# Performance work log

Measured on AMD Instinct MI355X. Metric: run time of the kernel, lower is better.

The kernel has to match this reference:

```python
import jax, jax.numpy as jnp
import numpy as np

N_NODES = 100000
N_EDGES = 3200000


def setup_inputs() -> dict:
    key = jax.random.key(0)
    ks = jax.random.split(key, 16)
    inp = {
        "noisy_coords": jax.random.normal(ks[0], (N_NODES, 3), dtype=jnp.float32),
        "atom_types": jax.random.randint(ks[1], (N_NODES,), 0, 2),
        "edge_index": jax.random.randint(ks[2], (2, N_EDGES), 0, N_NODES),
        "emb": jax.random.normal(ks[3], (2, 3), dtype=jnp.float32),
    }
    # GCNConv weights: 6->32->64->64->32->3 (hidden_dim=64)
    dims = [(6, 32), (32, 64), (64, 64), (64, 32), (32, 3)]
    for i, (din, dout) in enumerate(dims, start=1):
        inp[f"W{i}"] = jax.random.normal(ks[3 + i], (din, dout), dtype=jnp.float32) / np.sqrt(din).astype(np.float32)
        inp[f"b{i}"] = jnp.zeros((dout,), dtype=jnp.float32)
    return inp


def _gcn_conv(x, W, b, src, dst, norm, n):
    # GCNConv: X @ W, then symmetric-normalized scatter-add over edges, then bias.
    h = x @ W                       # [N, dout]
    msg = h[src] * norm[:, None]    # gather + edge normalization  [E+N, dout]
    return jax.ops.segment_sum(msg, dst, num_segments=n) + b


def reference(noisy_coords, atom_types, edge_index, emb,
              W1, b1, W2, b2, W3, b3, W4, b4, W5, b5):
    n = noisy_coords.shape[0]
    loop = jnp.arange(n)
    # PyG GCNConv adds self loops and uses deg^{-1/2} (A+I) deg^{-1/2} normalization
    src = jnp.concatenate([edge_index[0], loop])
    dst = jnp.concatenate([edge_index[1], loop])
    deg = jax.ops.segment_sum(jnp.ones(src.shape[0], dtype=jnp.float32), dst, num_segments=n)
    dinv = jnp.where(deg > 0, jax.lax.rsqrt(deg), 0.0)
    norm = dinv[src] * dinv[dst]    # [E+N]

    x = jnp.concatenate([noisy_coords, emb[atom_types]], axis=1)  # [N, 6]
    x = jax.nn.relu(_gcn_conv(x, W1, b1, src, dst, norm, n))
    x = jax.nn.relu(_gcn_conv(x, W2, b2, src, dst, norm, n))
    x = jax.nn.relu(_gcn_conv(x, W3, b3, src, dst, norm, n))
    x = jax.nn.relu(_gcn_conv(x, W4, b4, src, dst, norm, n))
    x = _gcn_conv(x, W5, b5, src, dst, norm, n)  # final layer: no relu
    return x
```

## Files before the change

kernel.cpp:

```cpp
#include <hip/hip_runtime.h>
#include <hip/hip_fp16.h>

#define NBLK_BIN 256
#define NBKT 196
#define BWIN 512
#define CAP 128


typedef unsigned int uint;

union U32H2 { uint u; __half2 h; };

__device__ inline float2 h2_to_f2(uint u) {
    U32H2 c; c.u = u;
    return __half22float2(c.h);
}
__device__ inline uint f2_to_h2(float a, float b) {
    U32H2 c; c.h = __floats2half2_rn(a, b);
    return c.u;
}

__global__ __launch_bounds__(1024) void bin_kernel(const int* __restrict__ src,
                                                   const int* __restrict__ dst,
                                                   uint* __restrict__ pairs,
                                                   int* __restrict__ blkcnt, int e) {
    __shared__ int lcnt[NBKT];
    int blk = blockIdx.x, tid = threadIdx.x;
    for (int t = tid; t < NBKT; t += 1024) lcnt[t] = 0;
    __syncthreads();
    int chunk = (e + NBLK_BIN - 1) / NBLK_BIN;
    int base = blk * chunk;
    int end = min(e, base + chunk);
    for (int i = base + tid; i < end; i += 1024) {
        int s = src[i], d = dst[i];
        int b = d >> 9;
        int pos = atomicAdd(&lcnt[b], 1);
        if (pos < CAP)
            pairs[((size_t)blk * NBKT + b) * CAP + pos] = ((uint)s << 9) | ((uint)d & 511u);
    }
    __syncthreads();
    for (int t = tid; t < NBKT; t += 1024) blkcnt[blk * NBKT + t] = min(lcnt[t], CAP);
}

__global__ __launch_bounds__(1024) void fill_kernel(const uint* __restrict__ pairs,
                                                    const int* __restrict__ blkcnt,
                                                    int* __restrict__ srcs,
                                                    int* __restrict__ cnt,
                                                    int* __restrict__ rowptr,
                                                    float* __restrict__ dinv, int n) {
    __shared__ int lc[BWIN];
    __shared__ int ps[BWIN];
    __shared__ int sm[NBLK_BIN];
    __shared__ int gbase_s;
    int b = blockIdx.x, tid = threadIdx.x;
    if (tid < BWIN) lc[tid] = 0;
    for (int t = tid; t < NBLK_BIN; t += 1024) sm[t] = blkcnt[t * NBKT + b];
    if (tid == 0) gbase_s = 0;
    __syncthreads();
    {
        long long tot = (long long)NBLK_BIN * b;
        int lsum = 0;
        for (long long j = tid; j < tot; j += 1024) {
            int blk = (int)(j / b);
            int bp  = (int)(j - (long long)blk * b);
            lsum += blkcnt[blk * NBKT + bp];
        }
        for (int o = 32; o > 0; o >>= 1) lsum += __shfl_down(lsum, o, 64);
        if ((tid & 63) == 0 && lsum != 0) atomicAdd(&gbase_s, lsum);
    }
    int wave = tid >> 6, lane = tid & 63;
    for (int blk = wave; blk < NBLK_BIN; blk += 16) {
        int m = sm[blk];
        const uint* p = pairs + ((size_t)blk * NBKT + b) * CAP;
        for (int i = lane; i < m; i += 64) atomicAdd(&lc[p[i] & 511u], 1);
    }
    __syncthreads();
    int myc = (tid < BWIN) ? lc[tid] : 0;
    if (tid < BWIN) ps[tid] = myc;
    __syncthreads();
    for (int off = 1; off < BWIN; off <<= 1) {
        int t = 0;
        if (tid < BWIN && tid >= off) t = ps[tid - off];
        __syncthreads();
        if (tid < BWIN) ps[tid] += t;
        __syncthreads();
    }
    int gbase = gbase_s;
    if (tid < BWIN) {
        int ex = ps[tid] - myc;
        int vtx = (b << 9) + tid;
        if (vtx < n) {
            cnt[vtx] = myc;
            rowptr[vtx] = gbase + ex;
            dinv[vtx] = rsqrtf(1.0f + (float)myc);
        }
    }
    __syncthreads();
    if (tid < BWIN) lc[tid] = ps[tid] - myc;
    __syncthreads();
    for (int blk = wave; blk < NBLK_BIN; blk += 16) {
        int m = sm[blk];
        const uint* p = pairs + ((size_t)blk * NBKT + b) * CAP;
        for (int i = lane; i < m; i += 64) {
            uint e2 = p[i];
            int o = atomicAdd(&lc[e2 & 511u], 1);
            srcs[gbase + o] = (int)(e2 >> 9);
        }
    }
}


__global__ __launch_bounds__(256) void build_x0_h_kernel(const float* __restrict__ coords,
                                                         const int* __restrict__ at,
                                                         const float* __restrict__ emb,
                                                         const float* __restrict__ dinv,
                                                         uint* __restrict__ x, int n) {
    int v = blockIdx.x * 256 + threadIdx.x;
    if (v >= n) return;
    float dv = dinv[v];
    float c0 = coords[3 * v + 0] * dv;
    float c1 = coords[3 * v + 1] * dv;
    float c2 = coords[3 * v + 2] * dv;
    int t = at[v];
    float e0 = emb[3 * t + 0] * dv;
    float e1 = emb[3 * t + 1] * dv;
    float e2 = emb[3 * t + 2] * dv;
    uint* row = x + (size_t)v * 4;
    row[0] = f2_to_h2(c0, c1);
    row[1] = f2_to_h2(c2, e0);
    row[2] = f2_to_h2(e1, e2);
    row[3] = 0;
}

template <int TPN, bool HAS_BIAS, bool RELU>
__global__ __launch_bounds__(256) void agg_v4_kernel(const uint* __restrict__ in_,
                                                     const float* __restrict__ dinv,
                                                     const int* __restrict__ rowptr,
                                                     const int* __restrict__ cnt,
                                                     const int* __restrict__ srcs,
                                                     const float* __restrict__ bias,
                                                     uint* __restrict__ out_, int n) {
    const uint4* in = (const uint4*)in_;
    uint4* out = (uint4*)out_;
    int gid = blockIdx.x * 256 + threadIdx.x;
    int v = gid / TPN, q = gid % TPN;
    if (v >= n) return;
    float ax[4], ay[4];
    {
        uint4 s0 = in[(size_t)v * TPN + q];
        uint su[4] = {s0.x, s0.y, s0.z, s0.w};
#pragma unroll
        for (int u = 0; u < 4; ++u) { float2 f = h2_to_f2(su[u]); ax[u] = f.x; ay[u] = f.y; }
    }
    int start = rowptr[v];
    int len = cnt[v];
    int k = 0;
    for (; k + 8 <= len; k += 8) {
        int sA = srcs[start + k];
        int sB = srcs[start + k + 1];
        int sC = srcs[start + k + 2];
        int sD = srcs[start + k + 3];
        int sE = srcs[start + k + 4];
        int sF = srcs[start + k + 5];
        int sG = srcs[start + k + 6];
        int sH = srcs[start + k + 7];
        uint4 fA = in[(size_t)sA * TPN + q];
        uint4 fB = in[(size_t)sB * TPN + q];
        uint4 fC = in[(size_t)sC * TPN + q];
        uint4 fD = in[(size_t)sD * TPN + q];
        uint4 fE = in[(size_t)sE * TPN + q];
        uint4 fF = in[(size_t)sF * TPN + q];
        uint4 fG = in[(size_t)sG * TPN + q];
        uint4 fH = in[(size_t)sH * TPN + q];
        uint ua[4] = {fA.x, fA.y, fA.z, fA.w};
        uint ub[4] = {fB.x, fB.y, fB.z, fB.w};
        uint uc[4] = {fC.x, fC.y, fC.z, fC.w};
        uint ud[4] = {fD.x, fD.y, fD.z, fD.w};
        uint ue[4] = {fE.x, fE.y, fE.z, fE.w};
        uint uf[4] = {fF.x, fF.y, fF.z, fF.w};
        uint ug[4] = {fG.x, fG.y, fG.z, fG.w};
        uint uh[4] = {fH.x, fH.y, fH.z, fH.w};
#pragma unroll
        for (int u = 0; u < 4; ++u) {
            float2 a = h2_to_f2(ua[u]);
            float2 b = h2_to_f2(ub[u]);
            float2 c = h2_to_f2(uc[u]);
            float2 d = h2_to_f2(ud[u]);
            float2 e2 = h2_to_f2(ue[u]);
            float2 f = h2_to_f2(uf[u]);
            float2 g = h2_to_f2(ug[u]);
            float2 h = h2_to_f2(uh[u]);
            ax[u] += ((a.x + b.x) + (c.x + d.x)) + ((e2.x + f.x) + (g.x + h.x));
            ay[u] += ((a.y + b.y) + (c.y + d.y)) + ((e2.y + f.y) + (g.y + h.y));
        }
    }
    for (; k + 4 <= len; k += 4) {
        int sA = srcs[start + k];
        int sB = srcs[start + k + 1];
        int sC = srcs[start + k + 2];
        int sD = srcs[start + k + 3];
        uint4 fA = in[(size_t)sA * TPN + q];
        uint4 fB = in[(size_t)sB * TPN + q];
        uint4 fC = in[(size_t)sC * TPN + q];
        uint4 fD = in[(size_t)sD * TPN + q];
        uint ua[4] = {fA.x, fA.y, fA.z, fA.w};
        uint ub[4] = {fB.x, fB.y, fB.z, fB.w};
        uint uc[4] = {fC.x, fC.y, fC.z, fC.w};
        uint ud[4] = {fD.x, fD.y, fD.z, fD.w};
#pragma unroll
        for (int u = 0; u < 4; ++u) {
            float2 a = h2_to_f2(ua[u]);
            float2 b = h2_to_f2(ub[u]);
            float2 c = h2_to_f2(uc[u]);
            float2 d = h2_to_f2(ud[u]);
            ax[u] += (a.x + b.x) + (c.x + d.x);
            ay[u] += (a.y + b.y) + (c.y + d.y);
        }
    }
    for (; k < len; ++k) {
        int s = srcs[start + k];
        uint4 f = in[(size_t)s * TPN + q];
        uint uu[4] = {f.x, f.y, f.z, f.w};
#pragma unroll
        for (int u = 0; u < 4; ++u) { float2 t = h2_to_f2(uu[u]); ax[u] += t.x; ay[u] += t.y; }
    }
    float dv = dinv[v];
#pragma unroll
    for (int u = 0; u < 4; ++u) {
        ax[u] *= dv; ay[u] *= dv;
        if (HAS_BIAS) { ax[u] += bias[8 * q + 2 * u]; ay[u] += bias[8 * q + 2 * u + 1]; }
        if (RELU) { ax[u] = fmaxf(ax[u], 0.0f); ay[u] = fmaxf(ay[u], 0.0f); }
    }
    uint4 o;
    o.x = f2_to_h2(ax[0], ay[0]);
    o.y = f2_to_h2(ax[1], ay[1]);
    o.z = f2_to_h2(ax[2], ay[2]);
    o.w = f2_to_h2(ax[3], ay[3]);
    out[(size_t)v * TPN + q] = o;
}

__global__ __launch_bounds__(256) void agg_l4l5_kernel(const uint* __restrict__ in_,
                                                       const float* __restrict__ dinv,
                                                       const int* __restrict__ rowptr,
                                                       const int* __restrict__ cnt,
                                                       const int* __restrict__ srcs,
                                                       const float* __restrict__ b4,
                                                       const float* __restrict__ W5,
                                                       float* __restrict__ outf, int n) {
    const uint4* in = (const uint4*)in_;
    int gid = blockIdx.x * 256 + threadIdx.x;
    int v = gid >> 2, q = gid & 3;
    if (v >= n) return;
    float ax[4], ay[4];
    {
        uint4 s0 = in[(size_t)v * 4 + q];
        uint su[4] = {s0.x, s0.y, s0.z, s0.w};
#pragma unroll
        for (int u = 0; u < 4; ++u) { float2 f = h2_to_f2(su[u]); ax[u] = f.x; ay[u] = f.y; }
    }
    int start = rowptr[v];
    int len = cnt[v];
    int k = 0;
    for (; k + 8 <= len; k += 8) {
        int sA = srcs[start + k];
        int sB = srcs[start + k + 1];
        int sC = srcs[start + k + 2];
        int sD = srcs[start + k + 3];
        int sE = srcs[start + k + 4];
        int sF = srcs[start + k + 5];
        int sG = srcs[start + k + 6];
        int sH = srcs[start + k + 7];
        uint4 fA = in[(size_t)sA * 4 + q];
        uint4 fB = in[(size_t)sB * 4 + q];
        uint4 fC = in[(size_t)sC * 4 + q];
        uint4 fD = in[(size_t)sD * 4 + q];
        uint4 fE = in[(size_t)sE * 4 + q];
        uint4 fF = in[(size_t)sF * 4 + q];
        uint4 fG = in[(size_t)sG * 4 + q];
        uint4 fH = in[(size_t)sH * 4 + q];
        uint ua[4] = {fA.x, fA.y, fA.z, fA.w};
        uint ub[4] = {fB.x, fB.y, fB.z, fB.w};
        uint uc[4] = {fC.x, fC.y, fC.z, fC.w};
        uint ud[4] = {fD.x, fD.y, fD.z, fD.w};
        uint ue[4] = {fE.x, fE.y, fE.z, fE.w};
        uint uf[4] = {fF.x, fF.y, fF.z, fF.w};
        uint ug[4] = {fG.x, fG.y, fG.z, fG.w};
        uint uh[4] = {fH.x, fH.y, fH.z, fH.w};
#pragma unroll
        for (int u = 0; u < 4; ++u) {
            float2 a = h2_to_f2(ua[u]);
            float2 b = h2_to_f2(ub[u]);
            float2 c = h2_to_f2(uc[u]);
            float2 d = h2_to_f2(ud[u]);
            float2 e2 = h2_to_f2(ue[u]);
            float2 f = h2_to_f2(uf[u]);
            float2 g = h2_to_f2(ug[u]);
            float2 h = h2_to_f2(uh[u]);
            ax[u] += ((a.x + b.x) + (c.x + d.x)) + ((e2.x + f.x) + (g.x + h.x));
            ay[u] += ((a.y + b.y) + (c.y + d.y)) + ((e2.y + f.y) + (g.y + h.y));
        }
    }
    for (; k + 4 <= len; k += 4) {
        int sA = srcs[start + k];
        int sB = srcs[start + k + 1];
        int sC = srcs[start + k + 2];
        int sD = srcs[start + k + 3];
        uint4 fA = in[(size_t)sA * 4 + q];
        uint4 fB = in[(size_t)sB * 4 + q];
        uint4 fC = in[(size_t)sC * 4 + q];
        uint4 fD = in[(size_t)sD * 4 + q];
        uint ua[4] = {fA.x, fA.y, fA.z, fA.w};
        uint ub[4] = {fB.x, fB.y, fB.z, fB.w};
        uint uc[4] = {fC.x, fC.y, fC.z, fC.w};
        uint ud[4] = {fD.x, fD.y, fD.z, fD.w};
#pragma unroll
        for (int u = 0; u < 4; ++u) {
            float2 a = h2_to_f2(ua[u]);
            float2 b = h2_to_f2(ub[u]);
            float2 c = h2_to_f2(uc[u]);
            float2 d = h2_to_f2(ud[u]);
            ax[u] += (a.x + b.x) + (c.x + d.x);
            ay[u] += (a.y + b.y) + (c.y + d.y);
        }
    }
    for (; k < len; ++k) {
        int s = srcs[start + k];
        uint4 f = in[(size_t)s * 4 + q];
        uint uu[4] = {f.x, f.y, f.z, f.w};
#pragma unroll
        for (int u = 0; u < 4; ++u) { float2 t = h2_to_f2(uu[u]); ax[u] += t.x; ay[u] += t.y; }
    }
    float dv = dinv[v];
    float feat[8];
#pragma unroll
    for (int u = 0; u < 4; ++u) {
        float fx = ax[u] * dv + b4[8 * q + 2 * u];
        float fy = ay[u] * dv + b4[8 * q + 2 * u + 1];
        feat[2 * u]     = fmaxf(fx, 0.0f);
        feat[2 * u + 1] = fmaxf(fy, 0.0f);
    }
    float p0 = 0.f, p1 = 0.f, p2 = 0.f;
#pragma unroll
    for (int m = 0; m < 8; ++m) {
        int j = 8 * q + m;
        p0 = fmaf(feat[m], W5[j * 3 + 0], p0);
        p1 = fmaf(feat[m], W5[j * 3 + 1], p1);
        p2 = fmaf(feat[m], W5[j * 3 + 2], p2);
    }
#pragma unroll
    for (int m = 1; m < 4; m <<= 1) {
        p0 += __shfl_xor(p0, m, 4);
        p1 += __shfl_xor(p1, m, 4);
        p2 += __shfl_xor(p2, m, 4);
    }
    float o = (q == 0) ? p0 : (q == 1 ? p1 : (q == 2 ? p2 : 0.0f));
    outf[(size_t)v * 4 + q] = (q < 3) ? o * dv : 0.0f;
}

template <int DIN, int DOUT, int DOUTH2, bool HAS_BIAS, bool RELU, bool SCALE>
__global__ __launch_bounds__(256) void gemm_h_kernel(const uint* __restrict__ xin,
                                                     const float* __restrict__ W,
                                                     const float* __restrict__ bias,
                                                     const float* __restrict__ dinv,
                                                     uint* __restrict__ xout,
                                                     int istride_u, int ostride, int n) {
    __shared__ float wlds[DIN * DOUT];
    for (int i = threadIdx.x; i < DIN * DOUT; i += 256) wlds[i] = W[i];
    __syncthreads();
    int gid = blockIdx.x * 256 + threadIdx.x;
    int v = gid / DOUTH2, j2 = gid % DOUTH2;
    if (v >= n) return;
    int j1 = 2 * j2;
    const uint* xr = xin + (size_t)v * istride_u;
    float acc0 = 0.0f, acc1 = 0.0f;
#pragma unroll
    for (int ku = 0; ku < DIN / 2; ++ku) {
        float2 xf = h2_to_f2(xr[ku]);
        int k = 2 * ku;
        acc0 = fmaf(xf.x, wlds[k * DOUT + j1], acc0);
        acc0 = fmaf(xf.y, wlds[(k + 1) * DOUT + j1], acc0);
        if (j1 + 1 < DOUT) {
            acc1 = fmaf(xf.x, wlds[k * DOUT + j1 + 1], acc1);
            acc1 = fmaf(xf.y, wlds[(k + 1) * DOUT + j1 + 1], acc1);
        }
    }
    if (HAS_BIAS) {
        acc0 += bias[j1];
        if (j1 + 1 < DOUT) acc1 += bias[j1 + 1];
    }
    if (RELU) { acc0 = fmaxf(acc0, 0.0f); acc1 = fmaxf(acc1, 0.0f); }
    if (SCALE) { float dv = dinv[v]; acc0 *= dv; acc1 *= dv; }
    xout[(size_t)v * ostride + j2] = f2_to_h2(acc0, acc1);
}

#define G34_NODES 16
__global__ __launch_bounds__(256) void gemm34_kernel(const uint* __restrict__ xin,
                                                     const float* __restrict__ W3,
                                                     const float* __restrict__ b3,
                                                     const float* __restrict__ W4,
                                                     const float* __restrict__ dinv,
                                                     uint* __restrict__ xout,
                                                     int n) {
    __shared__ float4 w3c[16][64];
    __shared__ float4 w4c[16][32];
    __shared__ float4 hb4[16][17];
    for (int idx = threadIdx.x; idx < 16 * 64; idx += 256) {
        int kc = idx >> 6, c = idx & 63;
        w3c[kc][c] = make_float4(W3[(4 * kc + 0) * 64 + c], W3[(4 * kc + 1) * 64 + c],
                                 W3[(4 * kc + 2) * 64 + c], W3[(4 * kc + 3) * 64 + c]);
    }
    for (int idx = threadIdx.x; idx < 16 * 32; idx += 256) {
        int kc = idx >> 5, c = idx & 31;
        w4c[kc][c] = make_float4(W4[(4 * kc + 0) * 32 + c], W4[(4 * kc + 1) * 32 + c],
                                 W4[(4 * kc + 2) * 32 + c], W4[(4 * kc + 3) * 32 + c]);
    }
    __syncthreads();
    int i  = threadIdx.x >> 4;
    int j2 = threadIdx.x & 15;
    int v  = blockIdx.x * G34_NODES + i;
    bool ok = (v < n);

    float acc[4] = {0.f, 0.f, 0.f, 0.f};
    if (ok) {
        const uint4* xr = (const uint4*)(xin + (size_t)v * 32);
        for (int kb = 0; kb < 8; ++kb) {
            uint4 xa = xr[kb];
            float2 f0 = h2_to_f2(xa.x);
            float2 f1 = h2_to_f2(xa.y);
            float2 f2v = h2_to_f2(xa.z);
            float2 f3 = h2_to_f2(xa.w);
            float xf0 = f0.x, xf1 = f0.y, xf2 = f1.x, xf3 = f1.y;
            float xf4 = f2v.x, xf5 = f2v.y, xf6 = f3.x, xf7 = f3.y;
#pragma unroll
            for (int u = 0; u < 4; ++u) {
                int c = j2 + 16 * u;
                float4 wa = w3c[2 * kb][c];
                float4 wb = w3c[2 * kb + 1][c];
                acc[u] = fmaf(xf0, wa.x, acc[u]);
                acc[u] = fmaf(xf1, wa.y, acc[u]);
                acc[u] = fmaf(xf2, wa.z, acc[u]);
                acc[u] = fmaf(xf3, wa.w, acc[u]);
                acc[u] = fmaf(xf4, wb.x, acc[u]);
                acc[u] = fmaf(xf5, wb.y, acc[u]);
                acc[u] = fmaf(xf6, wb.z, acc[u]);
                acc[u] = fmaf(xf7, wb.w, acc[u]);
            }
        }
    }
#pragma unroll
    for (int u = 0; u < 4; ++u) {
        int c = j2 + 16 * u;
        float h = ok ? fmaxf(acc[u] + b3[c], 0.0f) : 0.0f;
        ((float*)hb4)[i * 68 + c] = h;
    }
    __syncthreads();

    float a0 = 0.f, a1 = 0.f;
#pragma unroll
    for (int kc = 0; kc < 16; ++kc) {
        float4 h4  = hb4[i][kc];
        float4 wlo = w4c[kc][j2];
        float4 whi = w4c[kc][j2 + 16];
        a0 = fmaf(h4.x, wlo.x, a0);
        a0 = fmaf(h4.y, wlo.y, a0);
        a0 = fmaf(h4.z, wlo.z, a0);
        a0 = fmaf(h4.w, wlo.w, a0);
        a1 = fmaf(h4.x, whi.x, a1);
        a1 = fmaf(h4.y, whi.y, a1);
        a1 = fmaf(h4.z, whi.z, a1);
        a1 = fmaf(h4.w, whi.w, a1);
    }
    if (ok) {
        float dv = dinv[v];
        __half* o = (__half*)(xout + (size_t)v * 16);
        o[j2]      = __float2half(a0 * dv);
        o[j2 + 16] = __float2half(a1 * dv);
    }
}

__global__ __launch_bounds__(256) void agg_f4_kernel(const float* __restrict__ in_,
                                                     const float* __restrict__ dinv,
                                                     const int* __restrict__ rowptr,
                                                     const int* __restrict__ cnt,
                                                     const int* __restrict__ srcs,
                                                     const float* __restrict__ b,
                                                     float* __restrict__ out, int n) {
    const float4* in = (const float4*)in_;
    int v = blockIdx.x * 256 + threadIdx.x;
    if (v >= n) return;
    float4 s = in[v];
    float a0 = s.x, a1 = s.y, a2 = s.z;
    int start = rowptr[v];
    int len = cnt[v];
    int k = 0;
    for (; k + 8 <= len; k += 8) {
        int sA = srcs[start + k];
        int sB = srcs[start + k + 1];
        int sC = srcs[start + k + 2];
        int sD = srcs[start + k + 3];
        int sE = srcs[start + k + 4];
        int sF = srcs[start + k + 5];
        int sG = srcs[start + k + 6];
        int sH = srcs[start + k + 7];
        float4 fA = in[sA];
        float4 fB = in[sB];
        float4 fC = in[sC];
        float4 fD = in[sD];
        float4 fE = in[sE];
        float4 fF = in[sF];
        float4 fG = in[sG];
        float4 fH = in[sH];
        a0 += ((fA.x + fB.x) + (fC.x + fD.x)) + ((fE.x + fF.x) + (fG.x + fH.x));
        a1 += ((fA.y + fB.y) + (fC.y + fD.y)) + ((fE.y + fF.y) + (fG.y + fH.y));
        a2 += ((fA.z + fB.z) + (fC.z + fD.z)) + ((fE.z + fF.z) + (fG.z + fH.z));
    }
    for (; k + 4 <= len; k += 4) {
        int sA = srcs[start + k];
        int sB = srcs[start + k + 1];
        int sC = srcs[start + k + 2];
        int sD = srcs[start + k + 3];
        float4 fA = in[sA];
        float4 fB = in[sB];
        float4 fC = in[sC];
        float4 fD = in[sD];
        a0 += (fA.x + fB.x) + (fC.x + fD.x);
        a1 += (fA.y + fB.y) + (fC.y + fD.y);
        a2 += (fA.z + fB.z) + (fC.z + fD.z);
    }
    for (; k < len; ++k) {
        float4 f = in[srcs[start + k]];
        a0 += f.x; a1 += f.y; a2 += f.z;
    }
    float dv = dinv[v];
    out[(size_t)v * 3 + 0] = a0 * dv + b[0];
    out[(size_t)v * 3 + 1] = a1 * dv + b[1];
    out[(size_t)v * 3 + 2] = a2 * dv + b[2];
}


extern "C" void kernel_launch(void* const* d_in, const int* in_sizes, int n_in,
                              void* d_out, int out_size, void* d_ws, size_t ws_size,
                              hipStream_t stream) {
    const float* coords = (const float*)d_in[0];
    const int* at       = (const int*)d_in[1];
    const int* ei       = (const int*)d_in[2];
    const float* emb    = (const float*)d_in[3];
    const float* W1 = (const float*)d_in[4];  const float* b1 = (const float*)d_in[5];
    const float* W2 = (const float*)d_in[6];  const float* b2 = (const float*)d_in[7];
    const float* W3 = (const float*)d_in[8];  const float* b3 = (const float*)d_in[9];
    const float* W4 = (const float*)d_in[10]; const float* b4 = (const float*)d_in[11];
    const float* W5 = (const float*)d_in[12]; const float* b5 = (const float*)d_in[13];
    float* out = (float*)d_out;

    const int n = in_sizes[0] / 3;
    const int e = in_sizes[2] / 2;
    const int* src = ei;
    const int* dst = ei + e;

    char* ws = (char*)d_ws;
    size_t off = 0;
    float* dinv   = (float*)(ws + off); off += (size_t)n * 4;
    int*   cnt    = (int*)(ws + off);   off += (size_t)n * 4;
    int*   rowptr = (int*)(ws + off);   off += (size_t)n * 4;
    int*   blkcnt = (int*)(ws + off);   off += (size_t)NBLK_BIN * NBKT * 4;
    int*   srcs   = (int*)(ws + off);   off += (size_t)e * 4;
    char*  alias  = ws + off;
    uint*  pairs  = (uint*)alias;
    uint*  A_h    = (uint*)alias;
    uint*  B_h    = A_h + (size_t)n * 32;
    float* B_f    = (float*)(B_h + (size_t)n * 32);

    int nb = (n + 255) / 256;

    bin_kernel<<<NBLK_BIN, 1024, 0, stream>>>(src, dst, pairs, blkcnt, e);
    fill_kernel<<<NBKT, 1024, 0, stream>>>(pairs, blkcnt, srcs, cnt, rowptr, dinv, n);

    build_x0_h_kernel<<<nb, 256, 0, stream>>>(coords, at, emb, dinv, A_h, n);

    auto blocks = [](long long threads) { return (int)((threads + 255) / 256); };

    agg_v4_kernel<1, false, false><<<blocks((long long)n), 256, 0, stream>>>(
        A_h, dinv, rowptr, cnt, srcs, nullptr, B_h, n);
    gemm_h_kernel<6, 32, 16, true, true, true><<<blocks((long long)n * 16), 256, 0, stream>>>(
        B_h, W1, b1, dinv, A_h, 4, 16, n);

    agg_v4_kernel<4, false, false><<<blocks((long long)n * 4), 256, 0, stream>>>(
        A_h, dinv, rowptr, cnt, srcs, nullptr, B_h, n);
    gemm_h_kernel<32, 64, 32, true, true, true><<<blocks((long long)n * 32), 256, 0, stream>>>(
        B_h, W2, b2, dinv, A_h, 16, 32, n);

    agg_v4_kernel<8, false, false><<<blocks((long long)n * 8), 256, 0, stream>>>(
        A_h, dinv, rowptr, cnt, srcs, nullptr, B_h, n);
    gemm34_kernel<<<(n + G34_NODES - 1) / G34_NODES, 256, 0, stream>>>(
        B_h, W3, b3, W4, dinv, A_h, n);

    agg_l4l5_kernel<<<blocks((long long)n * 4), 256, 0, stream>>>(
        A_h, dinv, rowptr, cnt, srcs, b4, W5, B_f, n);

    agg_f4_kernel<<<blocks((long long)n), 256, 0, stream>>>(
        B_f, dinv, rowptr, cnt, srcs, b5, out, n);
}
```

Baseline: 387.5 us.

## Sort nodes by degree with counting sort to balance aggregation wavefronts

Result: slower. 787.9 us (+103.3%).

```diff
diff --git a/kernel.cpp b/kernel.cpp
--- a/kernel.cpp
+++ b/kernel.cpp
@@ -5,6 +5,7 @@
 #define NBKT 196
 #define BWIN 512
 #define CAP 128
+#define DBINS 256
 
 
 typedef unsigned int uint;
@@ -107,6 +108,37 @@
             srcs[gbase + o] = (int)(e2 >> 9);
         }
     }
+}
+
+__global__ __launch_bounds__(256) void dhist_kernel(const int* __restrict__ cnt,
+                                                    int* __restrict__ hist, int n) {
+    int v = blockIdx.x * 256 + threadIdx.x;
+    if (v < n) atomicAdd(&hist[min(cnt[v], DBINS - 1)], 1);
+}
+
+__global__ __launch_bounds__(DBINS) void dscan_kernel(int* __restrict__ hist) {
+    __shared__ int tmp[DBINS];
+    int t = threadIdx.x;
+    int orig = hist[t];
+    tmp[t] = orig;
+    __syncthreads();
+    for (int off = 1; off < DBINS; off <<= 1) {
+        int add = (t >= off) ? tmp[t - off] : 0;
+        __syncthreads();
+        tmp[t] += add;
+        __syncthreads();
+    }
+    hist[t] = tmp[t] - orig;
+}
+
+__global__ __launch_bounds__(256) void dscatter_kernel(const int* __restrict__ cnt,
+                                                       int* __restrict__ cursor,
+                                                       int* __restrict__ perm, int n) {
+    int v = blockIdx.x * 256 + threadIdx.x;
+    if (v >= n) return;
+    int b = min(cnt[v], DBINS - 1);
+    int p = atomicAdd(&cursor[b], 1);
+    perm[p] = v;
 }
 
 
@@ -138,13 +170,15 @@
                                                      const int* __restrict__ rowptr,
                                                      const int* __restrict__ cnt,
                                                      const int* __restrict__ srcs,
+                                                     const int* __restrict__ perm,
                                                      const float* __restrict__ bias,
                                                      uint* __restrict__ out_, int n) {
     const uint4* in = (const uint4*)in_;
     uint4* out = (uint4*)out_;
     int gid = blockIdx.x * 256 + threadIdx.x;
-    int v = gid / TPN, q = gid % TPN;
-    if (v >= n) return;
+    int vi = gid / TPN, q = gid % TPN;
+    if (vi >= n) return;
+    int v = perm[vi];
     float ax[4], ay[4];
     {
         uint4 s0 = in[(size_t)v * TPN + q];
@@ -244,13 +278,15 @@
                                                        const int* __restrict__ rowptr,
                                                        const int* __restrict__ cnt,
                                                        const int* __restrict__ srcs,
+                                                       const int* __restrict__ perm,
                                                        const float* __restrict__ b4,
                                                        const float* __restrict__ W5,
                                                        float* __restrict__ outf, int n) {
     const uint4* in = (const uint4*)in_;
     int gid = blockIdx.x * 256 + threadIdx.x;
-    int v = gid >> 2, q = gid & 3;
-    if (v >= n) return;
+    int vi = gid >> 2, q = gid & 3;
+    if (vi >= n) return;
+    int v = perm[vi];
     float ax[4], ay[4];
     {
         uint4 s0 = in[(size_t)v * 4 + q];
@@ -483,11 +519,13 @@
                                                      const int* __restrict__ rowptr,
                                                      const int* __restrict__ cnt,
                                                      const int* __restrict__ srcs,
+                                                     const int* __restrict__ perm,
                                                      const float* __restrict__ b,
                                                      float* __restrict__ out, int n) {
     const float4* in = (const float4*)in_;
-    int v = blockIdx.x * 256 + threadIdx.x;
-    if (v >= n) return;
+    int vi = blockIdx.x * 256 + threadIdx.x;
+    if (vi >= n) return;
+    int v = perm[vi];
     float4 s = in[v];
     float a0 = s.x, a1 = s.y, a2 = s.z;
     int start = rowptr[v];
@@ -562,6 +600,8 @@
     float* dinv   = (float*)(ws + off); off += (size_t)n * 4;
     int*   cnt    = (int*)(ws + off);   off += (size_t)n * 4;
     int*   rowptr = (int*)(ws + off);   off += (size_t)n * 4;
+    int*   perm   = (int*)(ws + off);   off += (size_t)n * 4;
+    int*   dhist  = (int*)(ws + off);   off += (size_t)DBINS * 4;
     int*   blkcnt = (int*)(ws + off);   off += (size_t)NBLK_BIN * NBKT * 4;
     int*   srcs   = (int*)(ws + off);   off += (size_t)e * 4;
     char*  alias  = ws + off;
@@ -575,28 +615,33 @@
     bin_kernel<<<NBLK_BIN, 1024, 0, stream>>>(src, dst, pairs, blkcnt, e);
     fill_kernel<<<NBKT, 1024, 0, stream>>>(pairs, blkcnt, srcs, cnt, rowptr, dinv, n);
 
+    hipMemsetAsync(dhist, 0, DBINS * 4, stream);
+    dhist_kernel<<<nb, 256, 0, stream>>>(cnt, dhist, n);
+    dscan_kernel<<<1, DBINS, 0, stream>>>(dhist);
+    dscatter_kernel<<<nb, 256, 0, stream>>>(cnt, dhist, perm, n);
+
     build_x0_h_kernel<<<nb, 256, 0, stream>>>(coords, at, emb, dinv, A_h, n);
 
     auto blocks = [](long long threads) { return (int)((threads + 255) / 256); };
 
     agg_v4_kernel<1, false, false><<<blocks((long long)n), 256, 0, stream>>>(
-        A_h, dinv, rowptr, cnt, srcs, nullptr, B_h, n);
+        A_h, dinv, rowptr, cnt, srcs, perm, nullptr, B_h, n);
     gemm_h_kernel<6, 32, 16, true, true, true><<<blocks((long long)n * 16), 256, 0, stream>>>(
         B_h, W1, b1, dinv, A_h, 4, 16, n);
 
     agg_v4_kernel<4, false, false><<<blocks((long long)n * 4), 256, 0, stream>>>(
-        A_h, dinv, rowptr, cnt, srcs, nullptr, B_h, n);
+        A_h, dinv, rowptr, cnt, srcs, perm, nullptr, B_h, n);
     gemm_h_kernel<32, 64, 32, true, true, true><<<blocks((long long)n * 32), 256, 0, stream>>>(
         B_h, W2, b2, dinv, A_h, 16, 32, n);
 
     agg_v4_kernel<8, false, false><<<blocks((long long)n * 8), 256, 0, stream>>>(
-        A_h, dinv, rowptr, cnt, srcs, nullptr, B_h, n);
+        A_h, dinv, rowptr, cnt, srcs, perm, nullptr, B_h, n);
     gemm34_kernel<<<(n + G34_NODES - 1) / G34_NODES, 256, 0, stream>>>(
         B_h, W3, b3, W4, dinv, A_h, n);
 
     agg_l4l5_kernel<<<blocks((long long)n * 4), 256, 0, stream>>>(
-        A_h, dinv, rowptr, cnt, srcs, b4, W5, B_f, n);
+        A_h, dinv, rowptr, cnt, srcs, perm, b4, W5, B_f, n);
 
     agg_f4_kernel<<<blocks((long long)n), 256, 0, stream>>>(
-        B_f, dinv, rowptr, cnt, srcs, b5, out, n);
-}
+        B_f, dinv, rowptr, cnt, srcs, perm, b5, out, n);
+}
```
